# Kernel tuning notes

Hardware: AMD Instinct MI355X
Metric: run time of the kernel (lower is better)

The kernel has to match this reference:

```python
import jax, jax.numpy as jnp
import numpy as np

N_SEQ, MAX_LEN, H_DIM, N_CHAR = 8, 4096, 1024, 256


def setup_inputs() -> dict:
    key = jax.random.key(0)
    ks = jax.random.split(key, 10)
    n_char_ev = 32768
    L, E = 12, 16384
    char_i_seq = jax.random.randint(ks[0], (n_char_ev,), 0, N_SEQ)
    char_i_pos = jax.random.randint(ks[1], (n_char_ev,), 0, MAX_LEN)
    char_ids = jax.random.randint(ks[2], (n_char_ev,), 0, N_CHAR)
    grp_i_seq = jax.random.randint(ks[3], (L, E), 0, N_SEQ)
    grp_i_first = jax.random.randint(ks[4], (L, E), 0, MAX_LEN)
    grp_i_second = jax.random.randint(ks[5], (L, E), 0, MAX_LEN)
    grp_i_pos = jax.random.randint(ks[6], (L, E), 0, MAX_LEN)
    # Learned params: embedding table (std = 1/sqrt(h_dim)) and composer Linear(2h -> h)
    emb_char = jax.random.normal(ks[7], (N_CHAR, H_DIM), dtype=jnp.float32) * (1.0 / H_DIM ** 0.5)
    W = jax.random.normal(ks[8], (2 * H_DIM, H_DIM), dtype=jnp.float32) * (1.0 / (2 * H_DIM) ** 0.5)
    b = jnp.zeros((H_DIM,), dtype=jnp.float32)
    return {"char_i_seq": char_i_seq, "char_i_pos": char_i_pos, "char_ids": char_ids,
            "grp_i_seq": grp_i_seq, "grp_i_first": grp_i_first, "grp_i_second": grp_i_second,
            "grp_i_pos": grp_i_pos, "emb_char": emb_char, "W": W, "b": b}


def reference(char_i_seq, char_i_pos, char_ids, grp_i_seq, grp_i_first,
              grp_i_second, grp_i_pos, emb_char, W, b):
    # h_frag: [n_seq, max_len, h_dim]
    h = jnp.zeros((N_SEQ, MAX_LEN, H_DIM), dtype=emb_char.dtype)
    # Leaf characters: embedding lookup + scatter-add
    h = h.at[char_i_seq, char_i_pos].add(emb_char[char_ids])

    def composer(left, right):
        # tanh(Linear(concat(left, right))) : [E, 2h] @ [2h, h] -> [E, h]
        return jnp.tanh(jnp.concatenate([left, right], axis=-1) @ W + b)

    def level_step(h, idx):
        i_seq, i_first, i_second, i_pos = idx
        out = composer(h[i_seq, i_first], h[i_seq, i_second])  # gather -> compose
        return h.at[i_seq, i_pos].add(out), None                # scatter-add

    h, _ = jax.lax.scan(level_step, h, (grp_i_seq, grp_i_first, grp_i_second, grp_i_pos))
    h = h.at[:, 0].set(0.0)  # h_frag[:, 0].fill_(0)
    return h
```

## Files before the change

### kernel.cpp

```cpp
#include <hip/hip_runtime.h>

#define NS 8
#define ML 4096
#define HD 1024
#define K2 2048
#define NEV 32768
#define NLEV 12
#define NE 16384
#define NSLOT (NS * ML)
#define CAP 8
#define BK 64
#define NT (K2 / BK)
#define LDS_BYTES 131072

typedef __attribute__((ext_vector_type(8))) short bf16x8;
typedef __attribute__((ext_vector_type(4))) float f32x4;

typedef __attribute__((address_space(1))) const void cvoid_g;
typedef __attribute__((address_space(3))) void void_l;

static __device__ __forceinline__ void load_lds_16(const void* g, void* l) {
    __builtin_amdgcn_global_load_lds((cvoid_g*)g, (void_l*)l, 16, 0, 0);
}

static __device__ __forceinline__ unsigned short f2bf(float f) {
    unsigned u = __float_as_uint(f);
    unsigned r = (u + 0x7fffu + ((u >> 16) & 1u)) >> 16;
    return (unsigned short)r;
}

static __device__ __forceinline__ float fast_tanh(float x) {
    return 1.0f - 2.0f / (__expf(2.0f * x) + 1.0f);
}

__global__ void wt_kernel(const float* __restrict__ W, unsigned short* __restrict__ WbT) {
    __shared__ unsigned short tile[64][65];
    const int t = threadIdx.x;
    const int k0 = blockIdx.x * 64;
    const int n0 = blockIdx.y * 64;
#pragma unroll
    for (int i = 0; i < 16; i++) {
        int idx = i * 256 + t;
        int r = idx >> 6, c = idx & 63;
        tile[r][c] = f2bf(W[(size_t)(k0 + r) * HD + n0 + c]);
    }
    __syncthreads();
#pragma unroll
    for (int i = 0; i < 16; i++) {
        int idx = i * 256 + t;
        int r = idx >> 6, c = idx & 63;
        WbT[(size_t)(n0 + r) * K2 + k0 + c] = tile[c][r];
    }
}

__global__ void char_ticket(const int* __restrict__ cseq, const int* __restrict__ cpos,
                            int* __restrict__ counts, int* __restrict__ ticket,
                            int* __restrict__ evlist) {
    const int e = blockIdx.x * 256 + threadIdx.x;
    if (e >= NEV) return;
    const int slot = cseq[e] * ML + cpos[e];
    const int t = atomicAdd(&counts[slot], 1);
    ticket[e] = t;
    if (t < CAP) evlist[slot * CAP + t] = e;
}

__global__ void char_slot_sum(const int* __restrict__ counts, const int* __restrict__ evlist,
                              const int* __restrict__ cid, const float* __restrict__ emb,
                              float* __restrict__ h) {
    const int slot = blockIdx.x;
    const int t = threadIdx.x;
    int n = counts[slot];
    if (n > CAP) n = CAP;
    float4 acc = {0.f, 0.f, 0.f, 0.f};
    for (int i = 0; i < n; i++) {
        const int e = evlist[slot * CAP + i];
        const int id = cid[e];
        const float4 v = ((const float4*)(emb + (size_t)id * HD))[t];
        acc.x += v.x; acc.y += v.y; acc.z += v.z; acc.w += v.w;
    }
    ((float4*)(h + (size_t)slot * HD))[t] = acc;
}

__global__ void char_overflow(const int* __restrict__ cseq, const int* __restrict__ cpos,
                              const int* __restrict__ cid, const int* __restrict__ ticket,
                              const float* __restrict__ emb, float* __restrict__ h) {
    const int e0 = blockIdx.x * 128;
    const int t = threadIdx.x;
    for (int i = 0; i < 128; i++) {
        const int e = e0 + i;
        if (ticket[e] < CAP) continue;
        const int slot = cseq[e] * ML + cpos[e];
        const int id = cid[e];
        const float4 v = ((const float4*)(emb + (size_t)id * HD))[t];
        float* dst = h + (size_t)slot * HD + t * 4;
        atomicAdd(dst + 0, v.x);
        atomicAdd(dst + 1, v.y);
        atomicAdd(dst + 2, v.z);
        atomicAdd(dst + 3, v.w);
    }
}

__global__ void grp_count(const int* __restrict__ iseq, const int* __restrict__ ipos,
                          int* __restrict__ gcounts) {
    const int idx = blockIdx.x * 256 + threadIdx.x;
    if (idx >= NLEV * NE) return;
    const int lev = idx >> 14;
    atomicAdd(&gcounts[lev * NSLOT + iseq[idx] * ML + ipos[idx]], 1);
}

__global__ void grp_dup(const int* __restrict__ iseq, const int* __restrict__ ipos,
                        const int* __restrict__ gcounts, unsigned char* __restrict__ dup) {
    const int idx = blockIdx.x * 256 + threadIdx.x;
    if (idx >= NLEV * NE) return;
    const int lev = idx >> 14;
    dup[idx] = (gcounts[lev * NSLOT + iseq[idx] * ML + ipos[idx]] > 1) ? 1 : 0;
}

__global__ void gather_x(const float* __restrict__ h, const int* __restrict__ iseq,
                         const int* __restrict__ ifirst, const int* __restrict__ isecond,
                         unsigned short* __restrict__ X) {
    const int e = blockIdx.x;
    const int t = threadIdx.x;
    const int seq = iseq[e], f = ifirst[e], s = isecond[e];
    const float4 a = ((const float4*)(h + ((size_t)seq * ML + f) * HD))[t];
    const float4 b = ((const float4*)(h + ((size_t)seq * ML + s) * HD))[t];
    ushort4 pa, pb;
    pa.x = f2bf(a.x); pa.y = f2bf(a.y); pa.z = f2bf(a.z); pa.w = f2bf(a.w);
    pb.x = f2bf(b.x); pb.y = f2bf(b.y); pb.z = f2bf(b.z); pb.w = f2bf(b.w);
    *(ushort4*)(X + (size_t)e * K2 + t * 4) = pa;
    *(ushort4*)(X + (size_t)e * K2 + HD + t * 4) = pb;
}

__global__ __launch_bounds__(512, 2) void gemm_scatter(
    const unsigned short* __restrict__ X,
    const unsigned short* __restrict__ WbT,
    const float* __restrict__ bias,
    const int* __restrict__ iseq, const int* __restrict__ ipos,
    const unsigned char* __restrict__ dup,
    float* __restrict__ h) {
    extern __shared__ unsigned short lds[];
    const int t = threadIdx.x;
    const int lane = t & 63;
    const int w = t >> 6;
    const int wm = w >> 2;
    const int wn = (w & 3) * 64;
    const int fr = lane & 15, fq = lane >> 4;

    const int bid = blockIdx.x;
    const int xcd = bid & 7, bix = bid >> 3;
    const int row0 = ((xcd & 1) * 32 + bix) * 256;
    const int col0 = (xcd >> 1) * 256;

    const int tr = t >> 3;
    const int sp = (t & 7) ^ (tr & 7);
    const unsigned short* Asrc = X + (size_t)(row0 + tr) * K2 + sp * 8;
    const unsigned short* Bsrc = WbT + (size_t)(col0 + tr) * K2 + sp * 8;

    f32x4 acc[8][4];
#pragma unroll
    for (int i = 0; i < 8; i++)
#pragma unroll
        for (int j = 0; j < 4; j++) acc[i][j] = (f32x4){0.f, 0.f, 0.f, 0.f};

    {
        unsigned short* dA = lds;
        unsigned short* dB = lds + 16384;
#pragma unroll
        for (int i = 0; i < 4; i++)
            load_lds_16(Asrc + (size_t)(i * 64) * K2, &dA[(i * 512 + t) * 8]);
#pragma unroll
        for (int i = 0; i < 4; i++)
            load_lds_16(Bsrc + (size_t)(i * 64) * K2, &dB[(i * 512 + t) * 8]);
    }

    for (int kt = 0; kt < NT; kt++) {
        const int d = kt & 1;
        if (kt + 1 < NT) {
            unsigned short* dA = lds + (d ^ 1) * 32768;
            unsigned short* dB = dA + 16384;
            const size_t ko = (size_t)(kt + 1) * BK;
#pragma unroll
            for (int i = 0; i < 4; i++)
                load_lds_16(Asrc + (size_t)(i * 64) * K2 + ko, &dA[(i * 512 + t) * 8]);
#pragma unroll
            for (int i = 0; i < 4; i++)
                load_lds_16(Bsrc + (size_t)(i * 64) * K2 + ko, &dB[(i * 512 + t) * 8]);
            asm volatile("s_waitcnt vmcnt(8)" ::: "memory");
        } else {
            asm volatile("s_waitcnt vmcnt(0)" ::: "memory");
        }
        __builtin_amdgcn_s_barrier();
        asm volatile("" ::: "memory");

        const unsigned short* sA = lds + d * 32768;
        const unsigned short* sB = sA + 16384;
#pragma unroll
        for (int q = 0; q < 4; q++) {
            const int mh = (q & 1) * 64;
            const int nh = (q >> 1) * 32;
            bf16x8 af[2][4], bfr[2][2];
#pragma unroll
            for (int ks = 0; ks < 2; ks++) {
                const int qs = ((ks * 4 + fq) ^ (fr & 7)) * 8;
#pragma unroll
                for (int mt = 0; mt < 4; mt++)
                    af[ks][mt] = *(const bf16x8*)&sA[(wm * 128 + mh + mt * 16 + fr) * BK + qs];
#pragma unroll
                for (int nt = 0; nt < 2; nt++)
                    bfr[ks][nt] = *(const bf16x8*)&sB[(wn + nh + nt * 16 + fr) * BK + qs];
            }
            __builtin_amdgcn_s_setprio(1);
#pragma unroll
            for (int ks = 0; ks < 2; ks++)
#pragma unroll
                for (int mt = 0; mt < 4; mt++)
#pragma unroll
                    for (int nt = 0; nt < 2; nt++)
                        acc[(q & 1) * 4 + mt][(q >> 1) * 2 + nt] =
                            __builtin_amdgcn_mfma_f32_16x16x32_bf16(
                                af[ks][mt], bfr[ks][nt],
                                acc[(q & 1) * 4 + mt][(q >> 1) * 2 + nt], 0, 0, 0);
            __builtin_amdgcn_s_setprio(0);
        }
        asm volatile("" ::: "memory");
        __builtin_amdgcn_s_barrier();
    }

    float bv[4];
#pragma unroll
    for (int ni = 0; ni < 4; ni++) bv[ni] = bias[col0 + wn + ni * 16 + fr];
#pragma unroll
    for (int mi = 0; mi < 8; mi++) {
#pragma unroll
        for (int r = 0; r < 4; r++) {
            const int e = row0 + wm * 128 + mi * 16 + fq * 4 + r;
            const int seq = iseq[e], pos = ipos[e];
            float* hrow = h + ((size_t)seq * ML + pos) * HD + col0 + wn;
            if (dup[e]) {
#pragma unroll
                for (int ni = 0; ni < 4; ni++) {
                    float x = fast_tanh(acc[mi][ni][r] + bv[ni]);
                    atomicAdd(&hrow[ni * 16 + fr], x);
                }
            } else {
#pragma unroll
                for (int ni = 0; ni < 4; ni++) {
                    float x = fast_tanh(acc[mi][ni][r] + bv[ni]);
                    hrow[ni * 16 + fr] += x;
                }
            }
        }
    }
}

__global__ void zero_first(float* __restrict__ h) {
    const int t = blockIdx.x * 256 + threadIdx.x;
    const int seq = t >> 10, d = t & 1023;
    h[(size_t)seq * ML * HD + d] = 0.0f;
}

extern "C" void kernel_launch(void* const* d_in, const int* in_sizes, int n_in,
                              void* d_out, int out_size, void* d_ws, size_t ws_size,
                              hipStream_t stream) {
    const int* char_i_seq = (const int*)d_in[0];
    const int* char_i_pos = (const int*)d_in[1];
    const int* char_ids   = (const int*)d_in[2];
    const int* grp_i_seq    = (const int*)d_in[3];
    const int* grp_i_first  = (const int*)d_in[4];
    const int* grp_i_second = (const int*)d_in[5];
    const int* grp_i_pos    = (const int*)d_in[6];
    const float* emb = (const float*)d_in[7];
    const float* W   = (const float*)d_in[8];
    const float* b   = (const float*)d_in[9];
    float* h = (float*)d_out;

    unsigned short* WbT = (unsigned short*)d_ws;
    unsigned short* X   = (unsigned short*)((char*)d_ws + (8u << 20));
    int* counts = (int*)((char*)d_ws + (72u << 20));
    int* ticket = (int*)((char*)d_ws + (72u << 20) + (1u << 18));
    int* evlist = (int*)((char*)d_ws + (72u << 20) + (1u << 19));
    int* gcounts = (int*)((char*)d_ws + (74u << 20));
    unsigned char* gdup = (unsigned char*)((char*)d_ws + (76u << 20));

    static bool attr_done = false;
    if (!attr_done) {
        (void)hipFuncSetAttribute((const void*)gemm_scatter,
                                  hipFuncAttributeMaxDynamicSharedMemorySize, LDS_BYTES);
        attr_done = true;
    }

    hipMemsetAsync(counts, 0, NSLOT * sizeof(int), stream);
    hipMemsetAsync(gcounts, 0, (size_t)NLEV * NSLOT * sizeof(int), stream);
    wt_kernel<<<dim3(32, 16), 256, 0, stream>>>(W, WbT);
    char_ticket<<<NEV / 256, 256, 0, stream>>>(char_i_seq, char_i_pos, counts, ticket, evlist);
    char_slot_sum<<<NSLOT, 256, 0, stream>>>(counts, evlist, char_ids, emb, h);
    char_overflow<<<NEV / 128, 256, 0, stream>>>(char_i_seq, char_i_pos, char_ids, ticket, emb, h);
    grp_count<<<(NLEV * NE) / 256, 256, 0, stream>>>(grp_i_seq, grp_i_pos, gcounts);
    grp_dup<<<(NLEV * NE) / 256, 256, 0, stream>>>(grp_i_seq, grp_i_pos, gcounts, gdup);

    for (int lev = 0; lev < NLEV; lev++) {
        const int* iseq = grp_i_seq + lev * NE;
        const int* ifir = grp_i_first + lev * NE;
        const int* isec = grp_i_second + lev * NE;
        const int* ipos = grp_i_pos + lev * NE;
        gather_x<<<NE, 256, 0, stream>>>(h, iseq, ifir, isec, X);
        gemm_scatter<<<dim3(256), 512, LDS_BYTES, stream>>>(X, WbT, b, iseq, ipos,
                                                            gdup + lev * NE, h);
    }
    zero_first<<<32, 256, 0, stream>>>(h);
}
```

Baseline: 1.630 ms.

## Interleave next-tile global-to-LDS loads with MFMA quadrants and reuse fragments

Splits each K-tile iteration of the GEMM into four quadrant phases. Each phase issues part of the next tile's global_load_lds between its own barriers, so memory traffic overlaps compute instead of being issued in one burst. A and B fragments are now kept in registers and reused across quadrants (af0/af1, bf0/bf1) instead of being reloaded from LDS per quadrant, which cuts LDS reads. Waits use partial vmcnt counts tied to which buffer halves are needed. The cost is more barriers per iteration and higher register pressure from the extra fragments.

```diff
diff --git a/kernel.cpp b/kernel.cpp
--- a/kernel.cpp
+++ b/kernel.cpp
@@ -165,65 +165,137 @@
     {
         unsigned short* dA = lds;
         unsigned short* dB = lds + 16384;
-#pragma unroll
-        for (int i = 0; i < 4; i++)
-            load_lds_16(Asrc + (size_t)(i * 64) * K2, &dA[(i * 512 + t) * 8]);
-#pragma unroll
-        for (int i = 0; i < 4; i++)
-            load_lds_16(Bsrc + (size_t)(i * 64) * K2, &dB[(i * 512 + t) * 8]);
-    }
+        load_lds_16(Bsrc + (size_t)(0 * 64) * K2, &dB[(0 * 512 + t) * 8]);
+        load_lds_16(Bsrc + (size_t)(1 * 64) * K2, &dB[(1 * 512 + t) * 8]);
+        load_lds_16(Bsrc + (size_t)(2 * 64) * K2, &dB[(2 * 512 + t) * 8]);
+        load_lds_16(Bsrc + (size_t)(3 * 64) * K2, &dB[(3 * 512 + t) * 8]);
+        load_lds_16(Asrc + (size_t)(0 * 64) * K2, &dA[(0 * 512 + t) * 8]);
+        load_lds_16(Asrc + (size_t)(2 * 64) * K2, &dA[(2 * 512 + t) * 8]);
+        load_lds_16(Asrc + (size_t)(1 * 64) * K2, &dA[(1 * 512 + t) * 8]);
+        load_lds_16(Asrc + (size_t)(3 * 64) * K2, &dA[(3 * 512 + t) * 8]);
+        asm volatile("s_waitcnt vmcnt(2)" ::: "memory");
+    }
+    __builtin_amdgcn_s_barrier();
+    asm volatile("" ::: "memory");
 
     for (int kt = 0; kt < NT; kt++) {
         const int d = kt & 1;
-        if (kt + 1 < NT) {
-            unsigned short* dA = lds + (d ^ 1) * 32768;
-            unsigned short* dB = dA + 16384;
-            const size_t ko = (size_t)(kt + 1) * BK;
-#pragma unroll
-            for (int i = 0; i < 4; i++)
-                load_lds_16(Asrc + (size_t)(i * 64) * K2 + ko, &dA[(i * 512 + t) * 8]);
-#pragma unroll
-            for (int i = 0; i < 4; i++)
-                load_lds_16(Bsrc + (size_t)(i * 64) * K2 + ko, &dB[(i * 512 + t) * 8]);
-            asm volatile("s_waitcnt vmcnt(8)" ::: "memory");
-        } else {
-            asm volatile("s_waitcnt vmcnt(0)" ::: "memory");
-        }
-        __builtin_amdgcn_s_barrier();
-        asm volatile("" ::: "memory");
-
         const unsigned short* sA = lds + d * 32768;
         const unsigned short* sB = sA + 16384;
-#pragma unroll
-        for (int q = 0; q < 4; q++) {
-            const int mh = (q & 1) * 64;
-            const int nh = (q >> 1) * 32;
-            bf16x8 af[2][4], bfr[2][2];
-#pragma unroll
-            for (int ks = 0; ks < 2; ks++) {
-                const int qs = ((ks * 4 + fq) ^ (fr & 7)) * 8;
-#pragma unroll
-                for (int mt = 0; mt < 4; mt++)
-                    af[ks][mt] = *(const bf16x8*)&sA[(wm * 128 + mh + mt * 16 + fr) * BK + qs];
+        unsigned short* nA = lds + (d ^ 1) * 32768;
+        unsigned short* nB = nA + 16384;
+        const size_t ko = (size_t)(kt + 1) * BK;
+        const bool st = (kt + 1 < NT);
+
+        bf16x8 af0[2][4], af1[2][4], bf0[2][2], bf1[2][2];
+
+#pragma unroll
+        for (int ks = 0; ks < 2; ks++) {
+            const int qs = ((ks * 4 + fq) ^ (fr & 7)) * 8;
+#pragma unroll
+            for (int mt = 0; mt < 4; mt++)
+                af0[ks][mt] = *(const bf16x8*)&sA[(wm * 128 + mt * 16 + fr) * BK + qs];
+#pragma unroll
+            for (int nt = 0; nt < 2; nt++)
+                bf0[ks][nt] = *(const bf16x8*)&sB[(wn + nt * 16 + fr) * BK + qs];
+        }
+        if (st) {
+            load_lds_16(Bsrc + (size_t)(0 * 64) * K2 + ko, &nB[(0 * 512 + t) * 8]);
+            load_lds_16(Bsrc + (size_t)(1 * 64) * K2 + ko, &nB[(1 * 512 + t) * 8]);
+        }
+        asm volatile("" ::: "memory");
+        __builtin_amdgcn_s_barrier();
+        asm volatile("" ::: "memory");
+        __builtin_amdgcn_s_setprio(1);
+#pragma unroll
+        for (int ks = 0; ks < 2; ks++)
+#pragma unroll
+            for (int mt = 0; mt < 4; mt++)
 #pragma unroll
                 for (int nt = 0; nt < 2; nt++)
-                    bfr[ks][nt] = *(const bf16x8*)&sB[(wn + nh + nt * 16 + fr) * BK + qs];
-            }
-            __builtin_amdgcn_s_setprio(1);
-#pragma unroll
-            for (int ks = 0; ks < 2; ks++)
-#pragma unroll
-                for (int mt = 0; mt < 4; mt++)
-#pragma unroll
-                    for (int nt = 0; nt < 2; nt++)
-                        acc[(q & 1) * 4 + mt][(q >> 1) * 2 + nt] =
-                            __builtin_amdgcn_mfma_f32_16x16x32_bf16(
-                                af[ks][mt], bfr[ks][nt],
-                                acc[(q & 1) * 4 + mt][(q >> 1) * 2 + nt], 0, 0, 0);
-            __builtin_amdgcn_s_setprio(0);
-        }
-        asm volatile("" ::: "memory");
-        __builtin_amdgcn_s_barrier();
+                    acc[mt][nt] = __builtin_amdgcn_mfma_f32_16x16x32_bf16(
+                        af0[ks][mt], bf0[ks][nt], acc[mt][nt], 0, 0, 0);
+        __builtin_amdgcn_s_setprio(0);
+        asm volatile("" ::: "memory");
+        __builtin_amdgcn_s_barrier();
+        asm volatile("" ::: "memory");
+
+#pragma unroll
+        for (int ks = 0; ks < 2; ks++) {
+            const int qs = ((ks * 4 + fq) ^ (fr & 7)) * 8;
+#pragma unroll
+            for (int nt = 0; nt < 2; nt++)
+                bf1[ks][nt] = *(const bf16x8*)&sB[(wn + 32 + nt * 16 + fr) * BK + qs];
+        }
+        if (st) {
+            load_lds_16(Bsrc + (size_t)(2 * 64) * K2 + ko, &nB[(2 * 512 + t) * 8]);
+            load_lds_16(Bsrc + (size_t)(3 * 64) * K2 + ko, &nB[(3 * 512 + t) * 8]);
+        }
+        asm volatile("" ::: "memory");
+        __builtin_amdgcn_s_barrier();
+        asm volatile("" ::: "memory");
+        __builtin_amdgcn_s_setprio(1);
+#pragma unroll
+        for (int ks = 0; ks < 2; ks++)
+#pragma unroll
+            for (int mt = 0; mt < 4; mt++)
+#pragma unroll
+                for (int nt = 0; nt < 2; nt++)
+                    acc[mt][2 + nt] = __builtin_amdgcn_mfma_f32_16x16x32_bf16(
+                        af0[ks][mt], bf1[ks][nt], acc[mt][2 + nt], 0, 0, 0);
+        __builtin_amdgcn_s_setprio(0);
+        if (st) { asm volatile("s_waitcnt vmcnt(4)" ::: "memory"); }
+        else    { asm volatile("s_waitcnt vmcnt(0)" ::: "memory"); }
+        __builtin_amdgcn_s_barrier();
+        asm volatile("" ::: "memory");
+
+#pragma unroll
+        for (int ks = 0; ks < 2; ks++) {
+            const int qs = ((ks * 4 + fq) ^ (fr & 7)) * 8;
+#pragma unroll
+            for (int mt = 0; mt < 4; mt++)
+                af1[ks][mt] = *(const bf16x8*)&sA[(wm * 128 + 64 + mt * 16 + fr) * BK + qs];
+        }
+        if (st) {
+            load_lds_16(Asrc + (size_t)(0 * 64) * K2 + ko, &nA[(0 * 512 + t) * 8]);
+            load_lds_16(Asrc + (size_t)(2 * 64) * K2 + ko, &nA[(2 * 512 + t) * 8]);
+        }
+        asm volatile("" ::: "memory");
+        __builtin_amdgcn_s_barrier();
+        asm volatile("" ::: "memory");
+        __builtin_amdgcn_s_setprio(1);
+#pragma unroll
+        for (int ks = 0; ks < 2; ks++)
+#pragma unroll
+            for (int mt = 0; mt < 4; mt++)
+#pragma unroll
+                for (int nt = 0; nt < 2; nt++)
+                    acc[4 + mt][nt] = __builtin_amdgcn_mfma_f32_16x16x32_bf16(
+                        af1[ks][mt], bf0[ks][nt], acc[4 + mt][nt], 0, 0, 0);
+        __builtin_amdgcn_s_setprio(0);
+        asm volatile("" ::: "memory");
+        __builtin_amdgcn_s_barrier();
+        asm volatile("" ::: "memory");
+
+        if (st) {
+            load_lds_16(Asrc + (size_t)(1 * 64) * K2 + ko, &nA[(1 * 512 + t) * 8]);
+            load_lds_16(Asrc + (size_t)(3 * 64) * K2 + ko, &nA[(3 * 512 + t) * 8]);
+        }
+        asm volatile("" ::: "memory");
+        __builtin_amdgcn_s_setprio(1);
+#pragma unroll
+        for (int ks = 0; ks < 2; ks++)
+#pragma unroll
+            for (int mt = 0; mt < 4; mt++)
+#pragma unroll
+                for (int nt = 0; nt < 2; nt++)
+                    acc[4 + mt][2 + nt] = __builtin_amdgcn_mfma_f32_16x16x32_bf16(
+                        af1[ks][mt], bf1[ks][nt], acc[4 + mt][2 + nt], 0, 0, 0);
+        __builtin_amdgcn_s_setprio(0);
+        if (st) { asm volatile("s_waitcnt vmcnt(2)" ::: "memory"); }
+        else    { asm volatile("s_waitcnt vmcnt(0)" ::: "memory"); }
+        __builtin_amdgcn_s_barrier();
+        asm volatile("" ::: "memory");
     }
 
     float bv[4];
```

New measurement: 1.511 ms. 7.3% less time.
